# Optimization experiments

Hardware: AMD Instinct MI355X
Metric: run time of the kernel (lower is better)

## Reference

```python
import jax, jax.numpy as jnp
import numpy as np

N = 8192
NT = 85       # number of DFIRE atom types
BINS = 28     # distance bins, d/0.7 clamped to [0,27]
EXCLU = 2     # nbre_nt_exclu


def setup_inputs() -> dict:
    key = jax.random.key(0)
    k1, k2, k3, k4 = jax.random.split(key, 4)
    # coords scaled so pairwise distances span the 0..19.6A cutoff range
    coords = jax.random.normal(k1, (N, 3), dtype=jnp.float32) * 10.0
    res_ids = jnp.sort(jax.random.randint(k2, (N,), 0, 400)).astype(jnp.int32)
    type_indices = jax.random.randint(k3, (N,), 0, NT).astype(jnp.int32)
    pot = jax.random.normal(k4, (NT, NT, BINS), dtype=jnp.float32)
    # original LUT is symmetric in the two type axes
    pot_tensor = 0.5 * (pot + jnp.transpose(pot, (1, 0, 2)))
    # upper-triangular pair indices, offset=1 (deterministic, like torch.triu_indices)
    ii, jj = np.triu_indices(N, 1)
    i_idx = jnp.asarray(ii, dtype=jnp.int32)
    j_idx = jnp.asarray(jj, dtype=jnp.int32)
    return {
        "coords": coords,
        "pot_tensor": pot_tensor,
        "res_ids": res_ids,
        "type_indices": type_indices,
        "i_idx": i_idx,
        "j_idx": j_idx,
    }


def reference(coords, pot_tensor, res_ids, type_indices, i_idx, j_idx):
    # sequence-separation and valid-type mask (stream compaction -> masked sum)
    sep = jnp.abs(res_ids[i_idx] - res_ids[j_idx])
    t1 = type_indices[i_idx]
    t2 = type_indices[j_idx]
    mask = (sep > EXCLU) & (t1 >= 0) & (t2 >= 0)

    # pairwise distances on all triu pairs
    diff = coords[i_idx] - coords[j_idx]              # [P,3]
    dists = jnp.sqrt(jnp.sum(diff * diff, axis=1)) + 1e-8  # [P]

    # bin + linear interpolation from the 3D LUT
    d_scaled = dists / 0.7
    d0 = jnp.floor(jnp.clip(d_scaled, 0.0, 27.0)).astype(jnp.int32)
    d1 = jnp.minimum(d0 + 1, 27)
    alpha = d_scaled - d0.astype(dists.dtype)

    # safe indices for masked-out pairs (their energy is multiplied by 0)
    t1s = jnp.where(mask, t1, 0)
    t2s = jnp.where(mask, t2, 0)
    e0 = pot_tensor[t1s, t2s, d0]
    e1 = pot_tensor[t1s, t2s, d1]
    energy = (1.0 - alpha) * e0 + alpha * e1

    w = mask & (dists < 19.6)
    return jnp.sum(energy * w.astype(energy.dtype))
```

## Files before the change

### kernel.cpp

```cpp
#include <hip/hip_runtime.h>

#define NT    85
#define BINS  28
#define NTB   (NT * BINS)
#define TILE  128

__global__ void repack_lut_k(const float* __restrict__ pot, float2* __restrict__ lut) {
    int idx = blockIdx.x * blockDim.x + threadIdx.x;
    const int total = NT * NT * BINS;
    if (idx >= total) return;
    int d  = idx % BINS;
    int ab = idx / BINS;
    int d1 = (d + 1 < BINS) ? d + 1 : BINS - 1;
    lut[idx] = make_float2(pot[idx], pot[ab * BINS + d1]);
}

__global__ __launch_bounds__(256) void hist_scan_k(const int* __restrict__ type,
                                                   int* __restrict__ offs, int N) {
    __shared__ int h[NT];
    for (int t = threadIdx.x; t < NT; t += 256) h[t] = 0;
    __syncthreads();
    for (int i = threadIdx.x; i < N; i += 256) atomicAdd(&h[type[i]], 1);
    __syncthreads();
    if (threadIdx.x == 0) {
        int s = 0;
        for (int t = 0; t < NT; ++t) { int c = h[t]; offs[t] = s; s += c; }
    }
}

__global__ void scatter_k(const float* __restrict__ coords, const int* __restrict__ res,
                          const int* __restrict__ type, int* __restrict__ offs,
                          float4* __restrict__ pc, int N) {
    int i = blockIdx.x * blockDim.x + threadIdx.x;
    if (i >= N) return;
    int t = type[i];
    int p = atomicAdd(&offs[t], 1);
    pc[p] = make_float4(coords[3 * i], coords[3 * i + 1], coords[3 * i + 2],
                        __int_as_float((t << 10) | res[i]));
}

__global__ __launch_bounds__(256) void dfire_pairs3(
    const float4* __restrict__ pc,
    const float2* __restrict__ lut,
    float* __restrict__ partial, int T) {

    __shared__ float4 jc[TILE];
    __shared__ float wsum[4];

    int k = blockIdx.x;
    int r = (int)((2.0 * T + 1.0 - sqrt((2.0 * T + 1.0) * (2.0 * T + 1.0) - 8.0 * (double)k)) * 0.5);
    if (r < 0) r = 0;
    if (r > T - 1) r = T - 1;
    while (r > 0 && (r * T - r * (r - 1) / 2) > k) --r;
    while (((r + 1) * T - (r + 1) * r / 2) <= k) ++r;
    int c = r + (k - (r * T - r * (r - 1) / 2));

    int bi = r * TILE, bj = c * TILE;
    int tid = threadIdx.x;

    if (tid < TILE) jc[tid] = pc[bj + tid];

    int ii = tid & (TILE - 1);
    float4 ci = pc[bi + ii];
    int wi   = __float_as_int(ci.w);
    int ires = wi & 1023;
    int itb  = (wi >> 10) * BINS;
    int ii_eff = (bi == bj) ? ii : -1;
    __syncthreads();

    float a0 = 0.f, a1 = 0.f, a2 = 0.f, a3 = 0.f;
    float a4 = 0.f, a5 = 0.f, a6 = 0.f, a7 = 0.f;
    int jj = tid >> 7;

#define STEP(J, ACC) do {                                              \
    float4 cj = jc[(J)];                                               \
    int   wj = __float_as_int(cj.w);                                   \
    float dx = ci.x - cj.x, dy = ci.y - cj.y, dz = ci.z - cj.z;        \
    float d2 = fmaf(dx, dx, fmaf(dy, dy, dz * dz));                    \
    int  sep = abs(ires - (wj & 1023));                                \
    bool v = (sep > 2) & (d2 < 19.6f * 19.6f) & ((J) > ii_eff);        \
    float dist  = __builtin_amdgcn_sqrtf(d2);                          \
    float ds    = dist * (1.0f / 0.7f);                                \
    float dsc   = fminf(ds, 27.0f);                                    \
    int   d0    = (int)dsc;                                            \
    float alpha = ds - (float)d0;                                      \
    int   base  = (wj >> 10) * NTB + itb + d0;                         \
    float2 e = lut[base];                                              \
    float en = fmaf(alpha, e.y - e.x, e.x);                            \
    ACC = fmaf(v ? 1.0f : 0.0f, en, ACC);                              \
} while (0)

    #pragma unroll
    for (int s = 0; s < TILE / 16; ++s, jj += 16) {
        STEP(jj,      a0);
        STEP(jj + 2,  a1);
        STEP(jj + 4,  a2);
        STEP(jj + 6,  a3);
        STEP(jj + 8,  a4);
        STEP(jj + 10, a5);
        STEP(jj + 12, a6);
        STEP(jj + 14, a7);
    }
#undef STEP

    float acc = ((a0 + a1) + (a2 + a3)) + ((a4 + a5) + (a6 + a7));
    for (int off = 32; off > 0; off >>= 1)
        acc += __shfl_down(acc, off, 64);
    if ((tid & 63) == 0) wsum[tid >> 6] = acc;
    __syncthreads();
    if (tid == 0) partial[blockIdx.x] = (wsum[0] + wsum[1]) + (wsum[2] + wsum[3]);
}

__global__ __launch_bounds__(256) void reduce_k(const float* __restrict__ p, int n,
                                                float* __restrict__ out) {
    __shared__ float ws[4];
    float a = 0.f;
    for (int i = threadIdx.x; i < n; i += 256) a += p[i];
    for (int off = 32; off > 0; off >>= 1)
        a += __shfl_down(a, off, 64);
    if ((threadIdx.x & 63) == 0) ws[threadIdx.x >> 6] = a;
    __syncthreads();
    if (threadIdx.x == 0) out[0] = (ws[0] + ws[1]) + (ws[2] + ws[3]);
}

__global__ __launch_bounds__(256) void dfire_pairs_fb(
    const float* __restrict__ coords, const int* __restrict__ res,
    const int* __restrict__ type, const float* __restrict__ pot,
    float* __restrict__ out, int T) {

    __shared__ float jx[TILE], jy[TILE], jz[TILE];
    __shared__ int   jres[TILE], jtype[TILE];

    int k = blockIdx.x;
    int r = (int)((2.0 * T + 1.0 - sqrt((2.0 * T + 1.0) * (2.0 * T + 1.0) - 8.0 * (double)k)) * 0.5);
    if (r < 0) r = 0;
    if (r > T - 1) r = T - 1;
    while (r > 0 && (r * T - r * (r - 1) / 2) > k) --r;
    while (((r + 1) * T - (r + 1) * r / 2) <= k) ++r;
    int c = r + (k - (r * T - r * (r - 1) / 2));

    int bi = r * TILE, bj = c * TILE;
    int tid = threadIdx.x;
    if (tid < TILE) {
        int gj = bj + tid;
        jx[tid] = coords[3 * gj]; jy[tid] = coords[3 * gj + 1]; jz[tid] = coords[3 * gj + 2];
        jres[tid] = res[gj]; jtype[tid] = type[gj];
    }
    int ii = tid & (TILE - 1);
    int gi = bi + ii;
    float ix = coords[3 * gi], iy = coords[3 * gi + 1], iz = coords[3 * gi + 2];
    int ires = res[gi], it = type[gi];
    int ii_eff = (bi == bj) ? ii : -1;
    __syncthreads();

    float acc = 0.f;
    int jj = tid >> 7;
    for (int s = 0; s < TILE / 2; ++s, jj += 2) {
        float dx = ix - jx[jj], dy = iy - jy[jj], dz = iz - jz[jj];
        float d2 = dx * dx + dy * dy + dz * dz;
        float dist = sqrtf(d2) + 1e-8f;
        int sep = abs(ires - jres[jj]);
        bool v = (sep > 2) & (dist < 19.6f) & (jj > ii_eff);
        if (v) {
            float ds = dist * (1.0f / 0.7f);
            int d0 = (int)fminf(ds, 27.0f);
            int d1 = (d0 + 1 < BINS) ? d0 + 1 : BINS - 1;
            float alpha = ds - (float)d0;
            int row = (jtype[jj] * NT + it) * BINS;
            float e0 = pot[row + d0], e1 = pot[row + d1];
            acc += e0 + alpha * (e1 - e0);
        }
    }
    for (int off = 32; off > 0; off >>= 1)
        acc += __shfl_down(acc, off, 64);
    if ((tid & 63) == 0) atomicAdd(out, acc);
}

extern "C" void kernel_launch(void* const* d_in, const int* in_sizes, int n_in,
                              void* d_out, int out_size, void* d_ws, size_t ws_size,
                              hipStream_t stream) {
    const float* coords = (const float*)d_in[0];
    const float* pot    = (const float*)d_in[1];
    const int*   res    = (const int*)d_in[2];
    const int*   type   = (const int*)d_in[3];

    const int N = in_sizes[2];
    const int T = N / TILE;
    const int nblk = T * (T + 1) / 2;

    float* out = (float*)d_out;

    const size_t lutBytes  = (size_t)NT * NT * BINS * sizeof(float2);
    const size_t pcBytes   = (size_t)N * sizeof(float4);
    const size_t offsBytes = 128 * sizeof(int);
    const size_t partBytes = (size_t)nblk * sizeof(float);
    const size_t need = lutBytes + pcBytes + offsBytes + partBytes;

    if (ws_size >= need) {
        char* w = (char*)d_ws;
        float2* lut     = (float2*)w;                     w += lutBytes;
        float4* pc      = (float4*)w;                     w += pcBytes;
        int*    offs    = (int*)w;                        w += offsBytes;
        float*  partial = (float*)w;

        const int total = NT * NT * BINS;
        repack_lut_k<<<(total + 255) / 256, 256, 0, stream>>>(pot, lut);
        hist_scan_k<<<1, 256, 0, stream>>>(type, offs, N);
        scatter_k<<<(N + 255) / 256, 256, 0, stream>>>(coords, res, type, offs, pc, N);
        dfire_pairs3<<<nblk, 256, 0, stream>>>(pc, lut, partial, T);
        reduce_k<<<1, 256, 0, stream>>>(partial, nblk, out);
    } else {
        hipMemsetAsync(out, 0, sizeof(float), stream);
        dfire_pairs_fb<<<nblk, 256, 0, stream>>>(coords, res, type, pot, out, T);
    }
}
```

Measured before the change: 278.1 us.

## Merge LUT repack and histogram kernels; read j-tile via scalar loads with branchy LUT

Fuses the LUT repack and type-histogram kernels into one launch, where the last block also does the histogram and scan. In the pair kernel, the shared-memory j tile and its barrier are removed. Each j coordinate is now read from global memory at a wave-uniform index via readfirstlane, so it can go through scalar loads. The LUT gather and interpolation now run only for valid pairs behind a branch, and the accumulators drop from eight to four. This risks wave divergence and a longer serial dependency chain in exchange for less LDS traffic and fewer wasted gathers.

```diff
diff --git a/kernel.cpp b/kernel.cpp
--- a/kernel.cpp
+++ b/kernel.cpp
@@ -4,27 +4,29 @@
 #define BINS  28
 #define NTB   (NT * BINS)
 #define TILE  128
-
-__global__ void repack_lut_k(const float* __restrict__ pot, float2* __restrict__ lut) {
-    int idx = blockIdx.x * blockDim.x + threadIdx.x;
-    const int total = NT * NT * BINS;
-    if (idx >= total) return;
-    int d  = idx % BINS;
-    int ab = idx / BINS;
-    int d1 = (d + 1 < BINS) ? d + 1 : BINS - 1;
-    lut[idx] = make_float2(pot[idx], pot[ab * BINS + d1]);
-}
-
-__global__ __launch_bounds__(256) void hist_scan_k(const int* __restrict__ type,
-                                                   int* __restrict__ offs, int N) {
-    __shared__ int h[NT];
-    for (int t = threadIdx.x; t < NT; t += 256) h[t] = 0;
-    __syncthreads();
-    for (int i = threadIdx.x; i < N; i += 256) atomicAdd(&h[type[i]], 1);
-    __syncthreads();
-    if (threadIdx.x == 0) {
-        int s = 0;
-        for (int t = 0; t < NT; ++t) { int c = h[t]; offs[t] = s; s += c; }
+#define LUT_ELEMS (NT * NT * BINS)
+
+__global__ __launch_bounds__(256) void prep_k(const float* __restrict__ pot,
+                                              const int* __restrict__ type, int N,
+                                              float2* __restrict__ lut,
+                                              int* __restrict__ offs) {
+    if ((int)blockIdx.x == (int)gridDim.x - 1) {
+        __shared__ int h[NT];
+        for (int t = threadIdx.x; t < NT; t += 256) h[t] = 0;
+        __syncthreads();
+        for (int i = threadIdx.x; i < N; i += 256) atomicAdd(&h[type[i]], 1);
+        __syncthreads();
+        if (threadIdx.x == 0) {
+            int s = 0;
+            for (int t = 0; t < NT; ++t) { int c = h[t]; offs[t] = s; s += c; }
+        }
+    }
+    int idx = blockIdx.x * 256 + threadIdx.x;
+    if (idx < LUT_ELEMS) {
+        int d  = idx % BINS;
+        int ab = idx / BINS;
+        int d1 = (d + 1 < BINS) ? d + 1 : BINS - 1;
+        lut[idx] = make_float2(pot[idx], pot[ab * BINS + d1]);
     }
 }
 
@@ -39,12 +41,11 @@
                         __int_as_float((t << 10) | res[i]));
 }
 
-__global__ __launch_bounds__(256) void dfire_pairs3(
+__global__ __launch_bounds__(256) void dfire_pairs4(
     const float4* __restrict__ pc,
     const float2* __restrict__ lut,
     float* __restrict__ partial, int T) {
 
-    __shared__ float4 jc[TILE];
     __shared__ float wsum[4];
 
     int k = blockIdx.x;
@@ -58,52 +59,47 @@
     int bi = r * TILE, bj = c * TILE;
     int tid = threadIdx.x;
 
-    if (tid < TILE) jc[tid] = pc[bj + tid];
-
     int ii = tid & (TILE - 1);
     float4 ci = pc[bi + ii];
     int wi   = __float_as_int(ci.w);
     int ires = wi & 1023;
     int itb  = (wi >> 10) * BINS;
     int ii_eff = (bi == bj) ? ii : -1;
-    __syncthreads();
 
     float a0 = 0.f, a1 = 0.f, a2 = 0.f, a3 = 0.f;
-    float a4 = 0.f, a5 = 0.f, a6 = 0.f, a7 = 0.f;
-    int jj = tid >> 7;
-
-#define STEP(J, ACC) do {                                              \
-    float4 cj = jc[(J)];                                               \
-    int   wj = __float_as_int(cj.w);                                   \
-    float dx = ci.x - cj.x, dy = ci.y - cj.y, dz = ci.z - cj.z;        \
-    float d2 = fmaf(dx, dx, fmaf(dy, dy, dz * dz));                    \
-    int  sep = abs(ires - (wj & 1023));                                \
-    bool v = (sep > 2) & (d2 < 19.6f * 19.6f) & ((J) > ii_eff);        \
-    float dist  = __builtin_amdgcn_sqrtf(d2);                          \
-    float ds    = dist * (1.0f / 0.7f);                                \
-    float dsc   = fminf(ds, 27.0f);                                    \
-    int   d0    = (int)dsc;                                            \
-    float alpha = ds - (float)d0;                                      \
-    int   base  = (wj >> 10) * NTB + itb + d0;                         \
-    float2 e = lut[base];                                              \
-    float en = fmaf(alpha, e.y - e.x, e.x);                            \
-    ACC = fmaf(v ? 1.0f : 0.0f, en, ACC);                              \
+    int j0 = tid >> 7;
+
+#define STEP(S, ACC) do {                                               \
+    int jjv = __builtin_amdgcn_readfirstlane(j0 + 2 * (S));             \
+    float4 cj = pc[bj + jjv];            \
+    int   wj   = __float_as_int(cj.w);                                  \
+    int   jres = wj & 1023;                                             \
+    int   jrow = (wj >> 10) * NTB;                                      \
+    float dx = ci.x - cj.x, dy = ci.y - cj.y, dz = ci.z - cj.z;         \
+    float d2 = fmaf(dx, dx, fmaf(dy, dy, dz * dz));                     \
+    int  sep = abs(ires - jres);                                        \
+    bool v = (sep > 2) & (d2 < 19.6f * 19.6f) & (jjv > ii_eff);         \
+    if (v) {                                                            \
+        float dist  = __builtin_amdgcn_sqrtf(d2);                       \
+        float ds    = dist * (1.0f / 0.7f);                             \
+        float dsc   = fminf(ds, 27.0f);                                 \
+        int   d0    = (int)dsc;                                         \
+        float alpha = ds - (float)d0;                                   \
+        float2 e = lut[jrow + itb + d0];                                \
+        ACC += fmaf(alpha, e.y - e.x, e.x);                             \
+    }                                                                   \
 } while (0)
 
     #pragma unroll
-    for (int s = 0; s < TILE / 16; ++s, jj += 16) {
-        STEP(jj,      a0);
-        STEP(jj + 2,  a1);
-        STEP(jj + 4,  a2);
-        STEP(jj + 6,  a3);
-        STEP(jj + 8,  a4);
-        STEP(jj + 10, a5);
-        STEP(jj + 12, a6);
-        STEP(jj + 14, a7);
+    for (int s = 0; s < TILE / 8; ++s) {
+        STEP(4 * s,     a0);
+        STEP(4 * s + 1, a1);
+        STEP(4 * s + 2, a2);
+        STEP(4 * s + 3, a3);
     }
 #undef STEP
 
-    float acc = ((a0 + a1) + (a2 + a3)) + ((a4 + a5) + (a6 + a7));
+    float acc = (a0 + a1) + (a2 + a3);
     for (int off = 32; off > 0; off >>= 1)
         acc += __shfl_down(acc, off, 64);
     if ((tid & 63) == 0) wsum[tid >> 6] = acc;
@@ -149,7 +145,7 @@
     int ii = tid & (TILE - 1);
     int gi = bi + ii;
     float ix = coords[3 * gi], iy = coords[3 * gi + 1], iz = coords[3 * gi + 2];
-    int ires = res[gi], it = type[gi];
+    int iresv = res[gi], it = type[gi];
     int ii_eff = (bi == bj) ? ii : -1;
     __syncthreads();
 
@@ -159,7 +155,7 @@
         float dx = ix - jx[jj], dy = iy - jy[jj], dz = iz - jz[jj];
         float d2 = dx * dx + dy * dy + dz * dz;
         float dist = sqrtf(d2) + 1e-8f;
-        int sep = abs(ires - jres[jj]);
+        int sep = abs(iresv - jres[jj]);
         bool v = (sep > 2) & (dist < 19.6f) & (jj > ii_eff);
         if (v) {
             float ds = dist * (1.0f / 0.7f);
@@ -190,7 +186,7 @@
 
     float* out = (float*)d_out;
 
-    const size_t lutBytes  = (size_t)NT * NT * BINS * sizeof(float2);
+    const size_t lutBytes  = (size_t)LUT_ELEMS * sizeof(float2);
     const size_t pcBytes   = (size_t)N * sizeof(float4);
     const size_t offsBytes = 128 * sizeof(int);
     const size_t partBytes = (size_t)nblk * sizeof(float);
@@ -203,11 +199,10 @@
         int*    offs    = (int*)w;                        w += offsBytes;
         float*  partial = (float*)w;
 
-        const int total = NT * NT * BINS;
-        repack_lut_k<<<(total + 255) / 256, 256, 0, stream>>>(pot, lut);
-        hist_scan_k<<<1, 256, 0, stream>>>(type, offs, N);
+        const int repackBlocks = (LUT_ELEMS + 255) / 256;
+        prep_k<<<repackBlocks + 1, 256, 0, stream>>>(pot, type, N, lut, offs);
         scatter_k<<<(N + 255) / 256, 256, 0, stream>>>(coords, res, type, offs, pc, N);
-        dfire_pairs3<<<nblk, 256, 0, stream>>>(pc, lut, partial, T);
+        dfire_pairs4<<<nblk, 256, 0, stream>>>(pc, lut, partial, T);
         reduce_k<<<1, 256, 0, stream>>>(partial, nblk, out);
     } else {
         hipMemsetAsync(out, 0, sizeof(float), stream);
```

Result: no change. 279.7 us (+0.6%).
